# Performance work log

Hardware: AMD Instinct MI355X
Metric: run time of the kernel (lower is better)

Reference implementation:

```python
import jax, jax.numpy as jnp
import numpy as np

DIM = 512
HEADS = 8
HEAD_DIM = DIM // HEADS
WINDOW = 128
TOKEN_SELF_ATTN_VALUE = -5e4  # lucidrains local-attention constant for shared_qk self mask


def setup_inputs() -> dict:
    key = jax.random.key(0)
    k1, k2, k3, k4 = jax.random.split(key, 4)
    B, N = 4, 8192
    x = jax.random.normal(k1, (B, N, DIM), dtype=jnp.float32)
    w_qkv = jax.random.normal(k2, (3 * DIM, DIM), dtype=jnp.float32) * (DIM ** -0.5)
    w_proj = jax.random.normal(k3, (DIM, DIM), dtype=jnp.float32) * (DIM ** -0.5)
    b_proj = jax.random.normal(k4, (DIM,), dtype=jnp.float32) * 0.01
    return {"x": x, "w_qkv": w_qkv, "w_proj": w_proj, "b_proj": b_proj}


def _look_around(b):
    # b: [B,H,nw,w,D] -> [B,H,nw,2w,D] = concat(prev_window, cur_window); window 0 padded with zeros
    padded = jnp.pad(b, ((0, 0), (0, 0), (1, 0), (0, 0), (0, 0)))
    return jnp.concatenate([padded[:, :, :-1], b], axis=3)


def _local_attn(q, k, v):
    # causal sliding-window attention, window=128, look_backward=1, shared_qk
    B, H, N, D = q.shape
    w = WINDOW
    nw = N // w
    scale = D ** -0.5
    # shared_qk: l2-normalize keys (F.normalize, eps=1e-12)
    k = k / jnp.clip(jnp.linalg.norm(k, axis=-1, keepdims=True), 1e-12, None)

    bq = q.reshape(B, H, nw, w, D)
    bk = _look_around(k.reshape(B, H, nw, w, D))  # [B,H,nw,2w,D]
    bv = _look_around(v.reshape(B, H, nw, w, D))

    t = jnp.arange(N).reshape(nw, w)
    t_pad = jnp.pad(t, ((1, 0), (0, 0)), constant_values=-1)
    bq_t = t                                         # [nw, w]
    bq_k = jnp.concatenate([t_pad[:-1], t], axis=1)  # [nw, 2w]

    sim = jnp.einsum('bhwie,bhwje->bhwij', bq, bk) * scale  # [B,H,nw,w,2w]

    self_mask = bq_t[:, :, None] == bq_k[:, None, :]
    causal_mask = bq_t[:, :, None] < bq_k[:, None, :]
    pad_mask = (bq_k == -1)[:, None, :]
    mask_value = -jnp.finfo(sim.dtype).max
    sim = jnp.where(self_mask, TOKEN_SELF_ATTN_VALUE, sim)
    sim = jnp.where(causal_mask | pad_mask, mask_value, sim)

    attn = jax.nn.softmax(sim, axis=-1)  # dropout is identity in eval mode
    out = jnp.einsum('bhwij,bhwje->bhwie', attn, bv)
    return out.reshape(B, H, N, D)


def reference(x, w_qkv, w_proj, b_proj):
    B, N, C = x.shape
    qkv = x @ w_qkv.T  # [B,N,3C]
    q, k, v = jnp.split(qkv, 3, axis=-1)
    to_heads = lambda t: t.reshape(B, N, HEADS, HEAD_DIM).transpose(0, 2, 1, 3)
    out = _local_attn(to_heads(q), to_heads(k), to_heads(v))  # [B,H,N,D]
    out = out.transpose(0, 2, 1, 3).reshape(B, N, C)
    return out @ w_proj.T + b_proj
```

## Files before the change

### kernel.cpp

```cpp
#include <hip/hip_runtime.h>
#include <stdint.h>

typedef uint16_t u16;
typedef __bf16 bf16x8 __attribute__((ext_vector_type(8)));
typedef float f32x4 __attribute__((ext_vector_type(4)));
typedef uint16_t u16x4 __attribute__((ext_vector_type(4)));
typedef uint16_t u16x8 __attribute__((ext_vector_type(8)));

typedef __attribute__((address_space(1))) void as1_void;
typedef __attribute__((address_space(3))) void as3_void;

__device__ __forceinline__ float bf2f(u16 b) {
    union { uint32_t u; float f; } v; v.u = ((uint32_t)b) << 16; return v.f;
}
__device__ __forceinline__ u16 f2bf(float f) {
    union { float f; uint32_t u; } v; v.f = f;
    uint32_t u = v.u;
    u += 0x7fffu + ((u >> 16) & 1u);
    return (u16)(u >> 16);
}
__device__ __forceinline__ void gload_lds16(const u16* g, u16* l) {
    __builtin_amdgcn_global_load_lds((as1_void*)g, (as3_void*)l, 16, 0, 0);
}

__global__ __launch_bounds__(256) void cvt_f32_bf16(const float* __restrict__ in,
                                                    u16* __restrict__ out, int n)
{
    int i = (blockIdx.x * 256 + threadIdx.x) * 8;
    const int stride = gridDim.x * 256 * 8;
    for (; i < n; i += stride) {
        f32x4 a = *(const f32x4*)(in + i);
        f32x4 b = *(const f32x4*)(in + i + 4);
        u16x8 o;
        o[0] = f2bf(a[0]); o[1] = f2bf(a[1]); o[2] = f2bf(a[2]); o[3] = f2bf(a[3]);
        o[4] = f2bf(b[0]); o[5] = f2bf(b[1]); o[6] = f2bf(b[2]); o[7] = f2bf(b[3]);
        *(u16x8*)(out + i) = o;
    }
}

template<bool C_F32, bool NORMK>
__global__ __launch_bounds__(256) void gemm_bt_bf16(
    const u16* __restrict__ A, int lda,
    const u16* __restrict__ B, int ldb,
    const float* __restrict__ bias,
    void* __restrict__ Cv, int ldc,
    int K)
{
    __shared__ u16 lA[128 * 32];
    __shared__ u16 lB[128 * 32];

    const int tid  = threadIdx.x;
    const int lane = tid & 63;
    const int wave = tid >> 6;
    const int wr   = (wave >> 1) * 64;
    const int wc   = (wave & 1) * 64;

    int fid = blockIdx.y * gridDim.x + blockIdx.x;
    const int nwg = gridDim.x * gridDim.y;
    if ((nwg & 7) == 0) fid = (fid & 7) * (nwg >> 3) + (fid >> 3);
    const int bx = fid % gridDim.x;
    const int by = fid / gridDim.x;
    const int row0 = by * 128;
    const int col0 = bx * 128;

    f32x4 acc[4][4] = {};

    for (int k0 = 0; k0 < K; k0 += 32) {
        #pragma unroll
        for (int i = 0; i < 2; ++i) {
            const int idx = i * 256 + tid;
            gload_lds16(A + (size_t)(row0 + (idx >> 2)) * lda + k0 + (idx & 3) * 8,
                        lA + (size_t)(i * 256 + wave * 64) * 8);
            gload_lds16(B + (size_t)(col0 + (idx >> 2)) * ldb + k0 + (idx & 3) * 8,
                        lB + (size_t)(i * 256 + wave * 64) * 8);
        }
        __syncthreads();

        bf16x8 af[4], bfv[4];
        #pragma unroll
        for (int m = 0; m < 4; ++m)
            af[m] = *(const bf16x8*)(lA + (wr + m * 16 + (lane & 15)) * 32 + (lane >> 4) * 8);
        #pragma unroll
        for (int n = 0; n < 4; ++n)
            bfv[n] = *(const bf16x8*)(lB + (wc + n * 16 + (lane & 15)) * 32 + (lane >> 4) * 8);
        #pragma unroll
        for (int m = 0; m < 4; ++m)
            #pragma unroll
            for (int n = 0; n < 4; ++n)
                acc[m][n] = __builtin_amdgcn_mfma_f32_16x16x32_bf16(af[m], bfv[n], acc[m][n], 0, 0, 0);
        __syncthreads();
    }

    if constexpr (NORMK) {
        if (col0 >= 512 && col0 < 1024) {
            #pragma unroll
            for (int m = 0; m < 4; ++m)
                #pragma unroll
                for (int j = 0; j < 4; ++j) {
                    float ss = 0.f;
                    #pragma unroll
                    for (int n = 0; n < 4; ++n) ss += acc[m][n][j] * acc[m][n][j];
                    ss += __shfl_xor(ss, 1);
                    ss += __shfl_xor(ss, 2);
                    ss += __shfl_xor(ss, 4);
                    ss += __shfl_xor(ss, 8);
                    const float scl = 1.f / fmaxf(sqrtf(ss), 1e-12f);
                    #pragma unroll
                    for (int n = 0; n < 4; ++n) acc[m][n][j] *= scl;
                }
        }
    }

    #pragma unroll
    for (int m = 0; m < 4; ++m) {
        const int r = row0 + wr + m * 16 + ((lane >> 4) << 2);
        #pragma unroll
        for (int n = 0; n < 4; ++n) {
            const int c = col0 + wc + n * 16 + (lane & 15);
            const float bv = bias ? bias[c] : 0.f;
            #pragma unroll
            for (int j = 0; j < 4; ++j) {
                const float val = acc[m][n][j] + bv;
                if constexpr (C_F32) ((float*)Cv)[(size_t)(r + j) * ldc + c] = val;
                else                 ((u16*)Cv)[(size_t)(r + j) * ldc + c] = f2bf(val);
            }
        }
    }
}

template<bool A_F32, bool C_F32, bool NORMK>
__global__ __launch_bounds__(256) void gemm_bt_f32(
    const void* __restrict__ Av, int lda,
    const float* __restrict__ B, int ldb,
    const float* __restrict__ bias,
    void* __restrict__ Cv, int ldc,
    int K)
{
    __shared__ u16 lA[128 * 32];
    __shared__ u16 lB[128 * 32];

    const int tid  = threadIdx.x;
    const int lane = tid & 63;
    const int wave = tid >> 6;
    const int wr   = (wave >> 1) * 64;
    const int wc   = (wave & 1) * 64;
    const int row0 = blockIdx.y * 128;
    const int col0 = blockIdx.x * 128;

    f32x4 acc[4][4] = {};

    for (int k0 = 0; k0 < K; k0 += 32) {
        #pragma unroll
        for (int i = 0; i < 4; ++i) {
            const int idx = i * 256 + tid;
            const int r = idx >> 3;
            const int p = (idx & 7) * 4;
            u16x4 a4, b4;
            if constexpr (A_F32) {
                const float* Af = (const float*)Av;
                f32x4 va = *(const f32x4*)(Af + (size_t)(row0 + r) * lda + k0 + p);
                a4[0] = f2bf(va[0]); a4[1] = f2bf(va[1]); a4[2] = f2bf(va[2]); a4[3] = f2bf(va[3]);
            } else {
                const u16* Ab = (const u16*)Av;
                a4 = *(const u16x4*)(Ab + (size_t)(row0 + r) * lda + k0 + p);
            }
            {
                f32x4 vb = *(const f32x4*)(B + (size_t)(col0 + r) * ldb + k0 + p);
                b4[0] = f2bf(vb[0]); b4[1] = f2bf(vb[1]); b4[2] = f2bf(vb[2]); b4[3] = f2bf(vb[3]);
            }
            *(u16x4*)&lA[r * 32 + p] = a4;
            *(u16x4*)&lB[r * 32 + p] = b4;
        }
        __syncthreads();

        bf16x8 af[4], bfv[4];
        #pragma unroll
        for (int m = 0; m < 4; ++m)
            af[m] = *(const bf16x8*)(lA + (wr + m * 16 + (lane & 15)) * 32 + (lane >> 4) * 8);
        #pragma unroll
        for (int n = 0; n < 4; ++n)
            bfv[n] = *(const bf16x8*)(lB + (wc + n * 16 + (lane & 15)) * 32 + (lane >> 4) * 8);
        #pragma unroll
        for (int m = 0; m < 4; ++m)
            #pragma unroll
            for (int n = 0; n < 4; ++n)
                acc[m][n] = __builtin_amdgcn_mfma_f32_16x16x32_bf16(af[m], bfv[n], acc[m][n], 0, 0, 0);
        __syncthreads();
    }

    if constexpr (NORMK) {
        if (col0 >= 512 && col0 < 1024) {
            #pragma unroll
            for (int m = 0; m < 4; ++m)
                #pragma unroll
                for (int j = 0; j < 4; ++j) {
                    float ss = 0.f;
                    #pragma unroll
                    for (int n = 0; n < 4; ++n) ss += acc[m][n][j] * acc[m][n][j];
                    ss += __shfl_xor(ss, 1);
                    ss += __shfl_xor(ss, 2);
                    ss += __shfl_xor(ss, 4);
                    ss += __shfl_xor(ss, 8);
                    const float scl = 1.f / fmaxf(sqrtf(ss), 1e-12f);
                    #pragma unroll
                    for (int n = 0; n < 4; ++n) acc[m][n][j] *= scl;
                }
        }
    }

    #pragma unroll
    for (int m = 0; m < 4; ++m) {
        const int r = row0 + wr + m * 16 + ((lane >> 4) << 2);
        #pragma unroll
        for (int n = 0; n < 4; ++n) {
            const int c = col0 + wc + n * 16 + (lane & 15);
            const float bv = bias ? bias[c] : 0.f;
            #pragma unroll
            for (int j = 0; j < 4; ++j) {
                const float val = acc[m][n][j] + bv;
                if constexpr (C_F32) ((float*)Cv)[(size_t)(r + j) * ldc + c] = val;
                else                 ((u16*)Cv)[(size_t)(r + j) * ldc + c] = f2bf(val);
            }
        }
    }
}

__global__ __launch_bounds__(512, 4) void attn_kernel(const u16* qkv, u16* o)
{
    constexpr int CC = 1536;
    constexpr int NTOK = 8192;
    constexpr int KP = 72;
    constexpr int VP = 136;
    constexpr int PP = 136;
    __shared__ u16 kn[128 * KP];
    __shared__ u16 vT[64 * VP];
    __shared__ u16 Pl[128 * PP];

    const int tid  = threadIdx.x;
    const int lane = tid & 63;
    const int wave = tid >> 6;
    const int cl = lane & 15;
    const int gr = lane >> 4;

    int blk = blockIdx.x;
    blk = (blk & 7) * (gridDim.x >> 3) + (blk >> 3);

    const int iw  = blk & 63;
    const int h   = (blk >> 6) & 7;
    const int b   = blk >> 9;

    const int tq0 = iw * 128;
    const size_t rowbase = (size_t)b * NTOK;
    const u16* qbase = qkv + rowbase * CC + h * 64;
    const u16* kbase = qbase + 512;
    const u16* vbase = qbase + 1024;

    const int wrow = wave * 16;
    bf16x8 qf[2];
    #pragma unroll
    for (int kk = 0; kk < 2; ++kk)
        qf[kk] = *(const bf16x8*)(qbase + (size_t)(tq0 + wrow + cl) * CC + kk * 32 + gr * 8);

    f32x4 oacc[4] = {};
    float m_run[4] = {-3.0e38f, -3.0e38f, -3.0e38f, -3.0e38f};
    float l_run[4] = {0.f, 0.f, 0.f, 0.f};

    for (int c = 0; c < 2; ++c) {
        const int tkc = tq0 - 128 + c * 128;

        #pragma unroll
        for (int p = 0; p < 2; ++p) {
            const int id = tid + p * 512;
            const int row = id >> 3, dc = id & 7;
            u16x8 v8 = {};
            if (tkc >= 0) v8 = *(const u16x8*)(kbase + (size_t)(tkc + row) * CC + dc * 8);
            *(u16x8*)&kn[row * KP + dc * 8] = v8;
        }
        #pragma unroll
        for (int p = 0; p < 2; ++p) {
            const int id = tid + p * 512;
            const int key = id & 127, dc = id >> 7;
            u16x8 v8 = {};
            if (tkc >= 0) v8 = *(const u16x8*)(vbase + (size_t)(tkc + key) * CC + dc * 8);
            #pragma unroll
            for (int e = 0; e < 8; ++e) vT[(dc * 8 + e) * VP + key] = v8[e];
        }
        __syncthreads();

        f32x4 s[8] = {};
        #pragma unroll
        for (int n = 0; n < 8; ++n)
            #pragma unroll
            for (int kk = 0; kk < 2; ++kk) {
                const bf16x8 kf = *(const bf16x8*)&kn[(n * 16 + cl) * KP + kk * 32 + gr * 8];
                s[n] = __builtin_amdgcn_mfma_f32_16x16x32_bf16(qf[kk], kf, s[n], 0, 0, 0);
            }

        float pmax[4] = {-3.0e38f, -3.0e38f, -3.0e38f, -3.0e38f};
        #pragma unroll
        for (int n = 0; n < 8; ++n) {
            const int tkk = tkc + n * 16 + cl;
            const bool pad = tkk < 0;
            #pragma unroll
            for (int j = 0; j < 4; ++j) {
                const int tq = tq0 + wrow + gr * 4 + j;
                float sv = s[n][j] * 0.125f;
                const int rel = tkk - tq;
                sv = (rel == 0) ? -5.0e4f : sv;
                sv = (rel > 0 || pad) ? -6.0e4f : sv;
                s[n][j] = sv;
                pmax[j] = fmaxf(pmax[j], sv);
            }
        }
        float cold[4];
        #pragma unroll
        for (int j = 0; j < 4; ++j) {
            pmax[j] = fmaxf(pmax[j], __shfl_xor(pmax[j], 1));
            pmax[j] = fmaxf(pmax[j], __shfl_xor(pmax[j], 2));
            pmax[j] = fmaxf(pmax[j], __shfl_xor(pmax[j], 4));
            pmax[j] = fmaxf(pmax[j], __shfl_xor(pmax[j], 8));
            const float mn = fmaxf(m_run[j], pmax[j]);
            cold[j] = __expf(m_run[j] - mn);
            m_run[j] = mn;
            l_run[j] *= cold[j];
        }
        #pragma unroll
        for (int n = 0; n < 8; ++n)
            #pragma unroll
            for (int j = 0; j < 4; ++j) {
                const float p = __expf(s[n][j] - m_run[j]);
                s[n][j] = p;
                l_run[j] += p;
            }
        #pragma unroll
        for (int n = 0; n < 4; ++n) {
            f32x4 t = oacc[n];
            t[0] *= cold[0]; t[1] *= cold[1]; t[2] *= cold[2]; t[3] *= cold[3];
            oacc[n] = t;
        }
        #pragma unroll
        for (int n = 0; n < 8; ++n)
            #pragma unroll
            for (int j = 0; j < 4; ++j)
                Pl[(wrow + gr * 4 + j) * PP + n * 16 + cl] = f2bf(s[n][j]);
        __syncthreads();

        #pragma unroll
        for (int kk = 0; kk < 4; ++kk) {
            const bf16x8 pa = *(const bf16x8*)&Pl[(wrow + cl) * PP + kk * 32 + gr * 8];
            #pragma unroll
            for (int n = 0; n < 4; ++n) {
                const bf16x8 vb = *(const bf16x8*)&vT[(n * 16 + cl) * VP + kk * 32 + gr * 8];
                oacc[n] = __builtin_amdgcn_mfma_f32_16x16x32_bf16(pa, vb, oacc[n], 0, 0, 0);
            }
        }
        __syncthreads();
    }

    float inv[4];
    #pragma unroll
    for (int j = 0; j < 4; ++j) {
        l_run[j] += __shfl_xor(l_run[j], 1);
        l_run[j] += __shfl_xor(l_run[j], 2);
        l_run[j] += __shfl_xor(l_run[j], 4);
        l_run[j] += __shfl_xor(l_run[j], 8);
        inv[j] = 1.f / l_run[j];
    }
    u16* obase = o + rowbase * CC + h * 64;
    const int r0 = tq0 + wrow + gr * 4;
    #pragma unroll
    for (int n = 0; n < 4; ++n) {
        const int d = n * 16 + cl;
        #pragma unroll
        for (int j = 0; j < 4; ++j)
            obase[(size_t)(r0 + j) * CC + d] = f2bf(oacc[n][j] * inv[j]);
    }
}

extern "C" void kernel_launch(void* const* d_in, const int* in_sizes, int n_in,
                              void* d_out, int out_size, void* d_ws, size_t ws_size,
                              hipStream_t stream)
{
    (void)in_sizes; (void)n_in; (void)out_size;
    const float* x      = (const float*)d_in[0];
    const float* w_qkv  = (const float*)d_in[1];
    const float* w_proj = (const float*)d_in[2];
    const float* b_proj = (const float*)d_in[3];
    float* out = (float*)d_out;

    const int BN = 4 * 8192;
    const size_t qkv_b = (size_t)BN * 1536 * 2;
    const size_t xb_b  = (size_t)BN * 512 * 2;
    const size_t wq_b  = (size_t)1536 * 512 * 2;
    const size_t wp_b  = (size_t)512 * 512 * 2;

    uint8_t* p = (uint8_t*)d_ws;
    u16* qkv = (u16*)p;

    if (ws_size >= qkv_b + xb_b + wq_b + wp_b) {
        u16* xb  = (u16*)(p + qkv_b);
        u16* wqb = (u16*)(p + qkv_b + xb_b);
        u16* wpb = (u16*)(p + qkv_b + xb_b + wq_b);
        cvt_f32_bf16<<<1024, 256, 0, stream>>>(x, xb, BN * 512);
        cvt_f32_bf16<<<96, 256, 0, stream>>>(w_qkv, wqb, 1536 * 512);
        cvt_f32_bf16<<<32, 256, 0, stream>>>(w_proj, wpb, 512 * 512);
        gemm_bt_bf16<false, true><<<dim3(12, BN / 128), 256, 0, stream>>>(
            xb, 512, wqb, 512, nullptr, qkv, 1536, 512);
        attn_kernel<<<dim3(4 * 8 * 64), 512, 0, stream>>>(qkv, qkv);
        gemm_bt_bf16<true, false><<<dim3(4, BN / 128), 256, 0, stream>>>(
            qkv, 1536, wpb, 512, b_proj, out, 512, 512);
    } else {
        gemm_bt_f32<true, false, true><<<dim3(12, BN / 128), 256, 0, stream>>>(
            x, 512, w_qkv, 512, nullptr, qkv, 1536, 512);
        attn_kernel<<<dim3(4 * 8 * 64), 512, 0, stream>>>(qkv, qkv);
        gemm_bt_f32<false, true, false><<<dim3(4, BN / 128), 256, 0, stream>>>(
            qkv, 1536, w_proj, 512, b_proj, out, 512, 512);
    }
}
```

Before: 200.9 us.

## Replace 128x128 bf16 GEMMs with double-buffered swizzled 256x256 tiles; merge conversions

Replaces the bf16 GEMM path with a new 512-thread kernel that computes 256x256 output tiles. It uses a 64-wide K step, two LDS buffers with an XOR-style chunk swizzle, explicit vmcnt waits, and raised MFMA priority, so global loads overlap compute and LDS bank conflicts drop. The three f32->bf16 conversion launches are merged into one kernel. The aim is better operand reuse and latency hiding in the QKV and output projections, at the cost of 128KB of LDS per block, one resident block per CU, and fewer blocks in the grid (256 blocks for the output GEMM).

```diff
diff --git a/kernel.cpp b/kernel.cpp
--- a/kernel.cpp
+++ b/kernel.cpp
@@ -23,25 +23,150 @@
     __builtin_amdgcn_global_load_lds((as1_void*)g, (as3_void*)l, 16, 0, 0);
 }
 
-__global__ __launch_bounds__(256) void cvt_f32_bf16(const float* __restrict__ in,
-                                                    u16* __restrict__ out, int n)
+__global__ __launch_bounds__(256) void cvt3(
+    const float* __restrict__ x,  u16* __restrict__ xb,
+    const float* __restrict__ wq, u16* __restrict__ wqb,
+    const float* __restrict__ wp, u16* __restrict__ wpb)
 {
-    int i = (blockIdx.x * 256 + threadIdx.x) * 8;
-    const int stride = gridDim.x * 256 * 8;
-    for (; i < n; i += stride) {
-        f32x4 a = *(const f32x4*)(in + i);
-        f32x4 b = *(const f32x4*)(in + i + 4);
+    const float* src; u16* dst; int base, nb;
+    const int b = blockIdx.x;
+    if (b < 1024)      { src = x;  dst = xb;  base = b;        nb = 1024; }
+    else if (b < 1072) { src = wq; dst = wqb; base = b - 1024; nb = 48;   }
+    else               { src = wp; dst = wpb; base = b - 1072; nb = 16;   }
+    size_t i = ((size_t)base * 256 + threadIdx.x) * 8;
+    const size_t stride = (size_t)nb * 256 * 8;
+    #pragma unroll
+    for (int it = 0; it < 8; ++it, i += stride) {
+        f32x4 a = *(const f32x4*)(src + i);
+        f32x4 c = *(const f32x4*)(src + i + 4);
         u16x8 o;
         o[0] = f2bf(a[0]); o[1] = f2bf(a[1]); o[2] = f2bf(a[2]); o[3] = f2bf(a[3]);
-        o[4] = f2bf(b[0]); o[5] = f2bf(b[1]); o[6] = f2bf(b[2]); o[7] = f2bf(b[3]);
-        *(u16x8*)(out + i) = o;
-    }
-}
-
-template<bool C_F32, bool NORMK>
-__global__ __launch_bounds__(256) void gemm_bt_bf16(
+        o[4] = f2bf(c[0]); o[5] = f2bf(c[1]); o[6] = f2bf(c[2]); o[7] = f2bf(c[3]);
+        *(u16x8*)(dst + i) = o;
+    }
+}
+
+template<int NT, bool C_F32, bool NORMK>
+__global__ __launch_bounds__(512) void gemm256(
     const u16* __restrict__ A, int lda,
     const u16* __restrict__ B, int ldb,
+    const float* __restrict__ bias,
+    void* __restrict__ Cv, int ldc)
+{
+    __shared__ u16 lA[2][256 * 64];
+    __shared__ u16 lB[2][256 * 64];
+
+    const int tid  = threadIdx.x;
+    const int lane = tid & 63;
+    const int wave = tid >> 6;
+    const int wm = wave >> 2;
+    const int wn = wave & 3;
+    const int cl = lane & 15;
+    const int gr = lane >> 4;
+
+    int fid = blockIdx.y * gridDim.x + blockIdx.x;
+    const int nwg = gridDim.x * gridDim.y;
+    fid = (fid & 7) * (nwg >> 3) + (fid >> 3);
+    const int row0 = (fid / gridDim.x) * 256;
+    const int col0 = (fid % gridDim.x) * 256;
+
+    const int srow   = lane >> 3;
+    const int schunk = ((lane & 7) - srow) & 7;
+
+    f32x4 acc[8][4] = {};
+
+    auto STAGE = [&](int t, int d) {
+        const int k0 = t * 64;
+        #pragma unroll
+        for (int i = 0; i < 4; ++i) {
+            const int Rg = wave * 32 + i * 8;
+            gload_lds16(A + (size_t)(row0 + Rg + srow) * lda + k0 + schunk * 8,
+                        &lA[d][Rg * 64]);
+            gload_lds16(B + (size_t)(col0 + Rg + srow) * ldb + k0 + schunk * 8,
+                        &lB[d][Rg * 64]);
+        }
+    };
+
+    auto COMPUTE = [&](int d) {
+        const u16* la = lA[d];
+        const u16* lb = lB[d];
+        bf16x8 bfrag[2][4];
+        #pragma unroll
+        for (int kk = 0; kk < 2; ++kk)
+            #pragma unroll
+            for (int n = 0; n < 4; ++n) {
+                const int rb = wn * 64 + n * 16 + cl;
+                bfrag[kk][n] = *(const bf16x8*)(lb + rb * 64 + (((kk * 4 + gr + rb) & 7) * 8));
+            }
+        __builtin_amdgcn_s_setprio(1);
+        #pragma unroll
+        for (int m = 0; m < 8; ++m) {
+            const int ra = wm * 128 + m * 16 + cl;
+            const bf16x8 a0 = *(const bf16x8*)(la + ra * 64 + (((gr + ra) & 7) * 8));
+            const bf16x8 a1 = *(const bf16x8*)(la + ra * 64 + (((4 + gr + ra) & 7) * 8));
+            #pragma unroll
+            for (int n = 0; n < 4; ++n)
+                acc[m][n] = __builtin_amdgcn_mfma_f32_16x16x32_bf16(a0, bfrag[0][n], acc[m][n], 0, 0, 0);
+            #pragma unroll
+            for (int n = 0; n < 4; ++n)
+                acc[m][n] = __builtin_amdgcn_mfma_f32_16x16x32_bf16(a1, bfrag[1][n], acc[m][n], 0, 0, 0);
+        }
+        __builtin_amdgcn_s_setprio(0);
+    };
+
+    STAGE(0, 0);
+    STAGE(1, 1);
+    #pragma unroll
+    for (int t = 0; t < NT; ++t) {
+        if (t < NT - 1) asm volatile("s_waitcnt vmcnt(8)" ::: "memory");
+        else            asm volatile("s_waitcnt vmcnt(0)" ::: "memory");
+        __builtin_amdgcn_s_barrier();
+        COMPUTE(t & 1);
+        __builtin_amdgcn_s_barrier();
+        if (t + 2 < NT) STAGE(t + 2, t & 1);
+    }
+
+    if constexpr (NORMK) {
+        if (col0 >= 512 && col0 < 1024) {
+            #pragma unroll
+            for (int m = 0; m < 8; ++m)
+                #pragma unroll
+                for (int j = 0; j < 4; ++j) {
+                    float ss = 0.f;
+                    #pragma unroll
+                    for (int n = 0; n < 4; ++n) ss += acc[m][n][j] * acc[m][n][j];
+                    ss += __shfl_xor(ss, 1);
+                    ss += __shfl_xor(ss, 2);
+                    ss += __shfl_xor(ss, 4);
+                    ss += __shfl_xor(ss, 8);
+                    const float scl = 1.f / fmaxf(sqrtf(ss), 1e-12f);
+                    #pragma unroll
+                    for (int n = 0; n < 4; ++n) acc[m][n][j] *= scl;
+                }
+        }
+    }
+
+    #pragma unroll
+    for (int m = 0; m < 8; ++m) {
+        const int r = row0 + wm * 128 + m * 16 + gr * 4;
+        #pragma unroll
+        for (int n = 0; n < 4; ++n) {
+            const int c = col0 + wn * 64 + n * 16 + cl;
+            const float bv = bias ? bias[c] : 0.f;
+            #pragma unroll
+            for (int j = 0; j < 4; ++j) {
+                const float val = acc[m][n][j] + bv;
+                if constexpr (C_F32) ((float*)Cv)[(size_t)(r + j) * ldc + c] = val;
+                else                 ((u16*)Cv)[(size_t)(r + j) * ldc + c] = f2bf(val);
+            }
+        }
+    }
+}
+
+template<bool A_F32, bool C_F32, bool NORMK>
+__global__ __launch_bounds__(256) void gemm_bt_f32(
+    const void* __restrict__ Av, int lda,
+    const float* __restrict__ B, int ldb,
     const float* __restrict__ bias,
     void* __restrict__ Cv, int ldc,
     int K)
@@ -54,25 +179,32 @@
     const int wave = tid >> 6;
     const int wr   = (wave >> 1) * 64;
     const int wc   = (wave & 1) * 64;
-
-    int fid = blockIdx.y * gridDim.x + blockIdx.x;
-    const int nwg = gridDim.x * gridDim.y;
-    if ((nwg & 7) == 0) fid = (fid & 7) * (nwg >> 3) + (fid >> 3);
-    const int bx = fid % gridDim.x;
-    const int by = fid / gridDim.x;
-    const int row0 = by * 128;
-    const int col0 = bx * 128;
+    const int row0 = blockIdx.y * 128;
+    const int col0 = blockIdx.x * 128;
 
     f32x4 acc[4][4] = {};
 
     for (int k0 = 0; k0 < K; k0 += 32) {
         #pragma unroll
-        for (int i = 0; i < 2; ++i) {
+        for (int i = 0; i < 4; ++i) {
             const int idx = i * 256 + tid;
-            gload_lds16(A + (size_t)(row0 + (idx >> 2)) * lda + k0 + (idx & 3) * 8,
-                        lA + (size_t)(i * 256 + wave * 64) * 8);
-            gload_lds16(B + (size_t)(col0 + (idx >> 2)) * ldb + k0 + (idx & 3) * 8,
-                        lB + (size_t)(i * 256 + wave * 64) * 8);
+            const int r = idx >> 3;
+            const int p = (idx & 7) * 4;
+            u16x4 a4, b4;
+            if constexpr (A_F32) {
+                const float* Af = (const float*)Av;
+                f32x4 va = *(const f32x4*)(Af + (size_t)(row0 + r) * lda + k0 + p);
+                a4[0] = f2bf(va[0]); a4[1] = f2bf(va[1]); a4[2] = f2bf(va[2]); a4[3] = f2bf(va[3]);
+            } else {
+                const u16* Ab = (const u16*)Av;
+                a4 = *(const u16x4*)(Ab + (size_t)(row0 + r) * lda + k0 + p);
+            }
+            {
+                f32x4 vb = *(const f32x4*)(B + (size_t)(col0 + r) * ldb + k0 + p);
+                b4[0] = f2bf(vb[0]); b4[1] = f2bf(vb[1]); b4[2] = f2bf(vb[2]); b4[3] = f2bf(vb[3]);
+            }
+            *(u16x4*)&lA[r * 32 + p] = a4;
+            *(u16x4*)&lB[r * 32 + p] = b4;
         }
         __syncthreads();
 
@@ -128,103 +260,6 @@
     }
 }
 
-template<bool A_F32, bool C_F32, bool NORMK>
-__global__ __launch_bounds__(256) void gemm_bt_f32(
-    const void* __restrict__ Av, int lda,
-    const float* __restrict__ B, int ldb,
-    const float* __restrict__ bias,
-    void* __restrict__ Cv, int ldc,
-    int K)
-{
-    __shared__ u16 lA[128 * 32];
-    __shared__ u16 lB[128 * 32];
-
-    const int tid  = threadIdx.x;
-    const int lane = tid & 63;
-    const int wave = tid >> 6;
-    const int wr   = (wave >> 1) * 64;
-    const int wc   = (wave & 1) * 64;
-    const int row0 = blockIdx.y * 128;
-    const int col0 = blockIdx.x * 128;
-
-    f32x4 acc[4][4] = {};
-
-    for (int k0 = 0; k0 < K; k0 += 32) {
-        #pragma unroll
-        for (int i = 0; i < 4; ++i) {
-            const int idx = i * 256 + tid;
-            const int r = idx >> 3;
-            const int p = (idx & 7) * 4;
-            u16x4 a4, b4;
-            if constexpr (A_F32) {
-                const float* Af = (const float*)Av;
-                f32x4 va = *(const f32x4*)(Af + (size_t)(row0 + r) * lda + k0 + p);
-                a4[0] = f2bf(va[0]); a4[1] = f2bf(va[1]); a4[2] = f2bf(va[2]); a4[3] = f2bf(va[3]);
-            } else {
-                const u16* Ab = (const u16*)Av;
-                a4 = *(const u16x4*)(Ab + (size_t)(row0 + r) * lda + k0 + p);
-            }
-            {
-                f32x4 vb = *(const f32x4*)(B + (size_t)(col0 + r) * ldb + k0 + p);
-                b4[0] = f2bf(vb[0]); b4[1] = f2bf(vb[1]); b4[2] = f2bf(vb[2]); b4[3] = f2bf(vb[3]);
-            }
-            *(u16x4*)&lA[r * 32 + p] = a4;
-            *(u16x4*)&lB[r * 32 + p] = b4;
-        }
-        __syncthreads();
-
-        bf16x8 af[4], bfv[4];
-        #pragma unroll
-        for (int m = 0; m < 4; ++m)
-            af[m] = *(const bf16x8*)(lA + (wr + m * 16 + (lane & 15)) * 32 + (lane >> 4) * 8);
-        #pragma unroll
-        for (int n = 0; n < 4; ++n)
-            bfv[n] = *(const bf16x8*)(lB + (wc + n * 16 + (lane & 15)) * 32 + (lane >> 4) * 8);
-        #pragma unroll
-        for (int m = 0; m < 4; ++m)
-            #pragma unroll
-            for (int n = 0; n < 4; ++n)
-                acc[m][n] = __builtin_amdgcn_mfma_f32_16x16x32_bf16(af[m], bfv[n], acc[m][n], 0, 0, 0);
-        __syncthreads();
-    }
-
-    if constexpr (NORMK) {
-        if (col0 >= 512 && col0 < 1024) {
-            #pragma unroll
-            for (int m = 0; m < 4; ++m)
-                #pragma unroll
-                for (int j = 0; j < 4; ++j) {
-                    float ss = 0.f;
-                    #pragma unroll
-                    for (int n = 0; n < 4; ++n) ss += acc[m][n][j] * acc[m][n][j];
-                    ss += __shfl_xor(ss, 1);
-                    ss += __shfl_xor(ss, 2);
-                    ss += __shfl_xor(ss, 4);
-                    ss += __shfl_xor(ss, 8);
-                    const float scl = 1.f / fmaxf(sqrtf(ss), 1e-12f);
-                    #pragma unroll
-                    for (int n = 0; n < 4; ++n) acc[m][n][j] *= scl;
-                }
-        }
-    }
-
-    #pragma unroll
-    for (int m = 0; m < 4; ++m) {
-        const int r = row0 + wr + m * 16 + ((lane >> 4) << 2);
-        #pragma unroll
-        for (int n = 0; n < 4; ++n) {
-            const int c = col0 + wc + n * 16 + (lane & 15);
-            const float bv = bias ? bias[c] : 0.f;
-            #pragma unroll
-            for (int j = 0; j < 4; ++j) {
-                const float val = acc[m][n][j] + bv;
-                if constexpr (C_F32) ((float*)Cv)[(size_t)(r + j) * ldc + c] = val;
-                else                 ((u16*)Cv)[(size_t)(r + j) * ldc + c] = f2bf(val);
-            }
-        }
-    }
-}
-
 __global__ __launch_bounds__(512, 4) void attn_kernel(const u16* qkv, u16* o)
 {
     constexpr int CC = 1536;
@@ -401,14 +436,12 @@
         u16* xb  = (u16*)(p + qkv_b);
         u16* wqb = (u16*)(p + qkv_b + xb_b);
         u16* wpb = (u16*)(p + qkv_b + xb_b + wq_b);
-        cvt_f32_bf16<<<1024, 256, 0, stream>>>(x, xb, BN * 512);
-        cvt_f32_bf16<<<96, 256, 0, stream>>>(w_qkv, wqb, 1536 * 512);
-        cvt_f32_bf16<<<32, 256, 0, stream>>>(w_proj, wpb, 512 * 512);
-        gemm_bt_bf16<false, true><<<dim3(12, BN / 128), 256, 0, stream>>>(
-            xb, 512, wqb, 512, nullptr, qkv, 1536, 512);
+        cvt3<<<1088, 256, 0, stream>>>(x, xb, w_qkv, wqb, w_proj, wpb);
+        gemm256<8, false, true><<<dim3(6, 128), 512, 0, stream>>>(
+            xb, 512, wqb, 512, nullptr, qkv, 1536);
         attn_kernel<<<dim3(4 * 8 * 64), 512, 0, stream>>>(qkv, qkv);
-        gemm_bt_bf16<true, false><<<dim3(4, BN / 128), 256, 0, stream>>>(
-            qkv, 1536, wpb, 512, b_proj, out, 512, 512);
+        gemm256<8, true, false><<<dim3(2, 128), 512, 0, stream>>>(
+            qkv, 1536, wpb, 512, b_proj, out, 512);
     } else {
         gemm_bt_f32<true, false, true><<<dim3(12, BN / 128), 256, 0, stream>>>(
             x, 512, w_qkv, 512, nullptr, qkv, 1536, 512);
```

New measurement: 186.4 us. -7.2%, faster.
